# Performance work log

Measured on AMD Instinct MI355X. Metric: run time of the kernel, lower is better.

The kernel has to match this reference:

```python
import jax, jax.numpy as jnp
import numpy as np

MAX_WAVELENGTH = 10000
BIG_NEG = -2.3819763e38

def _rope(x, positions):
    # x: [B, L, H, D], positions: [B, L] float32
    d = x.shape[-1]
    freq_exp = 2.0 / d * jnp.arange(d // 2, dtype=jnp.float32)
    timescale = MAX_WAVELENGTH ** freq_exp
    radians = (positions[..., None] / timescale[None, None, :])[..., None, :]  # [B,L,1,D/2]
    sin, cos = jnp.sin(radians), jnp.cos(radians)
    x1, x2 = jnp.split(x, 2, axis=-1)
    return jnp.concatenate([x1 * cos - x2 * sin, x2 * cos + x1 * sin], axis=-1).astype(x.dtype)

def _adaln_rmsnorm(x, cond, Wmod, bmod):
    # RMSNorm in fp32, then AdaLN scale/shift; returns (normed, gate[B,1,D])
    var = jnp.mean(jnp.square(x.astype(jnp.float32)), axis=-1, keepdims=True)
    normed = x * jax.lax.rsqrt(var + 1e-6)
    mod = (cond @ Wmod + bmod)[:, None, :]  # [B,1,3D]
    scale, shift, gate = jnp.split(mod, 3, axis=-1)
    return (normed * (1 + scale) + shift).astype(x.dtype), gate

def setup_inputs() -> dict:
    key = jax.random.key(0)
    ks = jax.random.split(key, 9)
    B, T, D, F, N, K, H = 2, 2048, 2048, 16384, 8, 1, 256
    x = jax.random.normal(ks[0], (B, T, D), jnp.float32)
    positions = jnp.broadcast_to(jnp.arange(T, dtype=jnp.float32), (B, T))
    attn_mask = jnp.broadcast_to(jnp.tril(jnp.ones((T, T), dtype=bool))[None, None], (B, 1, T, T))
    cond = jax.random.normal(ks[1], (B, D), jnp.float32)
    Wmod_a = jax.random.normal(ks[2], (D, 3 * D), jnp.float32) * 0.02
    bmod_a = jnp.zeros((3 * D,), jnp.float32)
    Wq = jax.random.normal(ks[3], (N, D, H), jnp.float32) * (D ** -0.5)
    Wkv = jax.random.normal(ks[4], (2, K, D, H), jnp.float32) * (D ** -0.5)
    Wo = jax.random.normal(ks[5], (N, H, D), jnp.float32) * ((N * H) ** -0.5)
    Wmod_f = jax.random.normal(ks[6], (D, 3 * D), jnp.float32) * 0.02
    bmod_f = jnp.zeros((3 * D,), jnp.float32)
    Wg = jax.random.normal(ks[7], (2, D, F), jnp.float32) * (D ** -0.5)
    Wl = jax.random.normal(ks[8], (F, D), jnp.float32) * (F ** -0.5)
    return dict(x=x, positions=positions, attn_mask=attn_mask, cond=cond,
                Wmod_a=Wmod_a, bmod_a=bmod_a, Wq=Wq, Wkv=Wkv, Wo=Wo,
                Wmod_f=Wmod_f, bmod_f=bmod_f, Wg=Wg, Wl=Wl)

def reference(x, positions, attn_mask, cond, Wmod_a, bmod_a, Wq, Wkv, Wo, Wmod_f, bmod_f, Wg, Wl):
    K = Wkv.shape[1]               # num_kv_heads
    H = Wq.shape[-1]               # head_dim
    # --- pre-attention AdaLN RMSNorm ---
    n, gate_a = _adaln_rmsnorm(x, cond, Wmod_a, bmod_a)
    # --- GQA projections ---
    q = jnp.einsum('BTD,NDH->BTNH', n, Wq)
    k = jnp.einsum('BSD,KDH->BSKH', n, Wkv[0])
    v = jnp.einsum('BSD,KDH->BSKH', n, Wkv[1])
    q = _rope(q, positions) * (H ** -0.5)
    k = _rope(k, positions)
    B, T, N, _ = q.shape
    q = q.reshape(B, T, K, N // K, H)  # B T K G H
    logits = jnp.einsum('BTKGH,BSKH->BKGTS', q, k, preferred_element_type=jnp.float32)
    masked = jnp.where(attn_mask[:, :, None, :, :], logits, BIG_NEG)
    probs = jax.nn.softmax(masked, axis=-1).astype(x.dtype)
    enc = jnp.einsum('BKGTS,BSKH->BTKGH', probs, v).reshape(B, T, N, H)
    attn_out = jnp.einsum('BTNH,NHD->BTD', enc, Wo)
    # gated residual
    x = x + attn_out * gate_a
    # --- pre-FFN AdaLN RMSNorm + gated-GeLU MLP ---
    n, gate_f = _adaln_rmsnorm(x, cond, Wmod_f, bmod_f)
    h = jax.nn.gelu(jnp.einsum('BTD,DF->BTF', n, Wg[0])) * jnp.einsum('BTD,DF->BTF', n, Wg[1])
    mlp_out = jnp.einsum('BTF,FD->BTD', h, Wl)
    return x + mlp_out * gate_f
```

## Files before the change

### kernel.cpp

```cpp
#include <hip/hip_runtime.h>
#include <hip/hip_bf16.h>

typedef __bf16 bf16_t;
typedef __bf16 bf16x8 __attribute__((ext_vector_type(8)));
typedef float  f32x4  __attribute__((ext_vector_type(4)));

#define DEV static __device__ __forceinline__

DEV void gload16(const bf16_t* g, bf16_t* l) {
    __builtin_amdgcn_global_load_lds(
        (const __attribute__((address_space(1))) void*)g,
        (__attribute__((address_space(3))) void*)l, 16, 0, 0);
}

enum { EPI_F32 = 0, EPI_BF16 = 1, EPI_RES = 2, EPI_GELU = 3, EPI_MUL = 4 };

#define G_MFMA(d, a, b) d = __builtin_amdgcn_mfma_f32_16x16x32_bf16(a, b, d, 0, 0, 0)

#define COMPUTE(AB0, AB1, BB0, BB1)                                           \
  { bf16x8 aF[8], bF[4];                                                      \
    _Pragma("unroll") for (int m8 = 0; m8 < 8; m8++)                          \
      aF[m8] = *(const bf16x8*)(AB0 + (m8 >> 2) * 4096 + (m8 & 3) * 1024);    \
    _Pragma("unroll") for (int nj = 0; nj < 4; nj++)                          \
      bF[nj] = *(const bf16x8*)(BB0 + nj * 1024);                             \
    _Pragma("unroll") for (int m8 = 0; m8 < 8; m8++)                          \
      _Pragma("unroll") for (int nj = 0; nj < 4; nj++)                        \
        G_MFMA(acc[m8][nj], aF[m8], bF[nj]);                                  \
    _Pragma("unroll") for (int m8 = 0; m8 < 8; m8++)                          \
      aF[m8] = *(const bf16x8*)(AB1 + (m8 >> 2) * 4096 + (m8 & 3) * 1024);    \
    _Pragma("unroll") for (int nj = 0; nj < 4; nj++)                          \
      bF[nj] = *(const bf16x8*)(BB1 + nj * 1024);                             \
    _Pragma("unroll") for (int m8 = 0; m8 < 8; m8++)                          \
      _Pragma("unroll") for (int nj = 0; nj < 4; nj++)                        \
        G_MFMA(acc[m8][nj], aF[m8], bF[nj]);                                  \
  }

#define STAGE8(kt, bi)                                                        \
  { SCA(kt, bi, 0); SCA(kt, bi, 1); SCA(kt, bi, 2); SCA(kt, bi, 3);           \
    SCB(kt, bi, 0); SCB(kt, bi, 1); SCB(kt, bi, 2); SCB(kt, bi, 3); }

template<int EPI>
__global__ __launch_bounds__(512, 1)
void gemma(const bf16_t* __restrict__ A, const bf16_t* __restrict__ Bt,
           void* __restrict__ Cout, int Kd, int lda, int ldb, int ldc,
           long sCz,
           const float* __restrict__ res, const float* __restrict__ gate,
           int gateStride, int rowsPerB, const bf16_t* __restrict__ aux)
{
    const int nbx = gridDim.x;
    const int nwg = nbx * gridDim.y;
    int lin = blockIdx.y * nbx + blockIdx.x;
    const int q8 = nwg >> 3, r8 = nwg & 7;
    const int xcd = lin & 7, oo = lin >> 3;
    lin = (xcd < r8 ? xcd * (q8 + 1) : r8 * (q8 + 1) + (xcd - r8) * q8) + oo;
    const long m0 = (long)(lin / nbx) * 256;
    const long n0 = (long)(lin % nbx) * 256;
    const long kb = (long)blockIdx.z * Kd;

    const int tid = threadIdx.x;
    const int l   = tid & 63;
    const int w   = tid >> 6;
    const int wr  = w >> 2;
    const int wcn = w & 3;

    __shared__ bf16_t sA[2][16384];
    __shared__ bf16_t sB[2][16384];

    const long sgc = (long)(((l & 7) ^ (l >> 3)) << 3);
    const int NT = Kd >> 6;
    const int NI = NT >> 1;

    const bf16_t* pA0 = A + (m0 + 0 * 64 + w * 8 + (l >> 3)) * (long)lda + kb + sgc;
    const bf16_t* pA1 = A + (m0 + 1 * 64 + w * 8 + (l >> 3)) * (long)lda + kb + sgc;
    const bf16_t* pA2 = A + (m0 + 2 * 64 + w * 8 + (l >> 3)) * (long)lda + kb + sgc;
    const bf16_t* pA3 = A + (m0 + 3 * 64 + w * 8 + (l >> 3)) * (long)lda + kb + sgc;
    const bf16_t* pB0 = Bt + (n0 + 0 * 64 + w * 8 + (l >> 3)) * (long)ldb + kb + sgc;
    const bf16_t* pB1 = Bt + (n0 + 1 * 64 + w * 8 + (l >> 3)) * (long)ldb + kb + sgc;
    const bf16_t* pB2 = Bt + (n0 + 2 * 64 + w * 8 + (l >> 3)) * (long)ldb + kb + sgc;
    const bf16_t* pB3 = Bt + (n0 + 3 * 64 + w * 8 + (l >> 3)) * (long)ldb + kb + sgc;

#define SCA(kt, bi, c) gload16(pA##c + (kt), &sA[bi][(c) * 4096 + w * 512])
#define SCB(kt, bi, c) gload16(pB##c + (kt), &sB[bi][(c) * 4096 + w * 512])

    f32x4 acc[8][4];
#pragma unroll
    for (int i = 0; i < 8; i++)
#pragma unroll
        for (int j = 0; j < 4; j++) acc[i][j] = f32x4{0.f, 0.f, 0.f, 0.f};

    const int co0 = ((l >> 4) ^ (l & 7)) << 3;
    const int co1 = ((4 + (l >> 4)) ^ (l & 7)) << 3;

    const bf16_t* rbA00 = &sA[0][(wr * 128 + (l & 15)) * 64 + co0];
    const bf16_t* rbA01 = &sA[0][(wr * 128 + (l & 15)) * 64 + co1];
    const bf16_t* rbA10 = &sA[1][(wr * 128 + (l & 15)) * 64 + co0];
    const bf16_t* rbA11 = &sA[1][(wr * 128 + (l & 15)) * 64 + co1];
    const bf16_t* rbB00 = &sB[0][(wcn * 64 + (l & 15)) * 64 + co0];
    const bf16_t* rbB01 = &sB[0][(wcn * 64 + (l & 15)) * 64 + co1];
    const bf16_t* rbB10 = &sB[1][(wcn * 64 + (l & 15)) * 64 + co0];
    const bf16_t* rbB11 = &sB[1][(wcn * 64 + (l & 15)) * 64 + co1];

    STAGE8(0, 0);

    for (int it = 0; it < NI; ++it) {
        const int v = 2 * it + 1;
        asm volatile("s_waitcnt lgkmcnt(0)" ::: "memory");
        __builtin_amdgcn_s_barrier();
        STAGE8((long)v * 64, 1);
        asm volatile("s_waitcnt vmcnt(8)" ::: "memory");
        __builtin_amdgcn_s_barrier();
        COMPUTE(rbA00, rbA01, rbB00, rbB01);
        asm volatile("s_waitcnt lgkmcnt(0)" ::: "memory");
        __builtin_amdgcn_s_barrier();
        if (v + 1 < NT) {
            STAGE8((long)(v + 1) * 64, 0);
            asm volatile("s_waitcnt vmcnt(8)" ::: "memory");
        } else {
            asm volatile("s_waitcnt vmcnt(0)" ::: "memory");
        }
        __builtin_amdgcn_s_barrier();
        COMPUTE(rbA10, rbA11, rbB10, rbB11);
    }

#pragma unroll
    for (int mi = 0; mi < 8; mi++) {
#pragma unroll
        for (int nj = 0; nj < 4; nj++) {
            f32x4 vv = acc[mi][nj];
            const long col   = n0 + wcn * 64 + nj * 16 + (l & 15);
            const long row0r = m0 + wr * 128 + mi * 16 + ((l >> 4) * 4);
#pragma unroll
            for (int e = 0; e < 4; e++) {
                const long row = row0r + e;
                const long idx = row * (long)ldc + col + (long)blockIdx.z * sCz;
                const float val = vv[e];
                if constexpr (EPI == EPI_F32) {
                    ((float*)Cout)[idx] = val;
                } else if constexpr (EPI == EPI_BF16) {
                    ((bf16_t*)Cout)[idx] = (bf16_t)val;
                } else if constexpr (EPI == EPI_RES) {
                    const int b = (int)(row / rowsPerB);
                    ((float*)Cout)[idx] = res[row * (long)ldc + col] + val * gate[(long)b * gateStride + col];
                } else if constexpr (EPI == EPI_GELU) {
                    const float gl = 0.5f * val * (1.f + tanhf(0.7978845608f * (val + 0.044715f * val * val * val)));
                    ((bf16_t*)Cout)[idx] = (bf16_t)gl;
                } else if constexpr (EPI == EPI_MUL) {
                    ((bf16_t*)Cout)[idx] = (bf16_t)((float)aux[idx] * val);
                }
            }
        }
    }
#undef SCA
#undef SCB
}

__global__ __launch_bounds__(256)
void combine_splitk(const float* __restrict__ P, const float* __restrict__ res,
                    const float* __restrict__ gate, float* __restrict__ out,
                    int D, int T, int gateStride, long zstride, long n4)
{
    for (long i4 = (long)blockIdx.x * 256 + threadIdx.x; i4 < n4; i4 += (long)gridDim.x * 256) {
        const long i = i4 * 4;
        const float4 p0 = *(const float4*)(P + i);
        const float4 p1 = *(const float4*)(P + i + zstride);
        const float4 xv = *(const float4*)(res + i);
        const long row = i / D;
        const int  b   = (int)(row / T);
        const int  col = (int)(i - row * D);
        const float* gp = gate + (long)b * gateStride + col;
        float4 r;
        r.x = xv.x + (p0.x + p1.x) * gp[0];
        r.y = xv.y + (p0.y + p1.y) * gp[1];
        r.z = xv.z + (p0.z + p1.z) * gp[2];
        r.w = xv.w + (p0.w + p1.w) * gp[3];
        *(float4*)(out + i) = r;
    }
}

template<int EPI, int CAUSAL>
__global__ __launch_bounds__(256)
void gemm_bt(const bf16_t* __restrict__ A, const bf16_t* __restrict__ Bt,
             void* __restrict__ Cout,
             int M, int N, int Kd, int lda, int ldb, int ldc,
             long sAz, long sBz, long sCz, long sCz2)
{
    const int tid = threadIdx.x;
    const int l   = tid & 63;
    const int w   = tid >> 6;
    const int wr  = w >> 1, wc = w & 1;
    const long m0 = (long)blockIdx.y * 128;
    const long n0 = (long)blockIdx.x * 128;
    const int  z  = blockIdx.z;

    if constexpr (CAUSAL == 1) {
        if (n0 > m0 + 127) return;
    }
    int kend = Kd;
    if constexpr (CAUSAL == 2) {
        const int kc = (int)m0 + 128;
        kend = kc < Kd ? kc : Kd;
    }

    A  += (long)z * sAz;
    Bt += (long)(z >> 3) * sBz;
    const long cOff = (long)(z >> 3) * sCz2 + (long)(z & 7) * sCz;

    __shared__ bf16_t As[128 * 32];
    __shared__ bf16_t Bs[128 * 32];

    const int srow = w * 16 + (l >> 2);
    const int scol = (l & 3) * 8;
    const bf16_t* Ag = A  + (m0 + srow) * (long)lda + scol;
    const bf16_t* Bg = Bt + (n0 + srow) * (long)ldb + scol;

    bf16_t* ldsA = As + w * 512;
    bf16_t* ldsB = Bs + w * 512;

    f32x4 acc[16];
    const f32x4 fz = {0.f, 0.f, 0.f, 0.f};
#pragma unroll
    for (int i = 0; i < 16; i++) acc[i] = fz;

    for (int k0 = 0; k0 < kend; k0 += 32) {
        gload16(Ag + k0,                  ldsA);
        gload16(Ag + k0 + 64 * (long)lda, ldsA + 2048);
        gload16(Bg + k0,                  ldsB);
        gload16(Bg + k0 + 64 * (long)ldb, ldsB + 2048);
        __syncthreads();

        bf16x8 af[4], bfr[4];
#pragma unroll
        for (int f = 0; f < 4; f++) {
            af[f]  = *(const bf16x8*)(As + (wr * 64 + f * 16 + (l & 15)) * 32 + (l >> 4) * 8);
            bfr[f] = *(const bf16x8*)(Bs + (wc * 64 + f * 16 + (l & 15)) * 32 + (l >> 4) * 8);
        }
#pragma unroll
        for (int i = 0; i < 4; i++)
#pragma unroll
            for (int j = 0; j < 4; j++)
                acc[i * 4 + j] = __builtin_amdgcn_mfma_f32_16x16x32_bf16(af[i], bfr[j], acc[i * 4 + j], 0, 0, 0);
        __syncthreads();
    }

#pragma unroll
    for (int i = 0; i < 4; i++) {
#pragma unroll
        for (int j = 0; j < 4; j++) {
            f32x4 v = acc[i * 4 + j];
            const long col  = n0 + wc * 64 + j * 16 + (l & 15);
            const long row0 = m0 + wr * 64 + i * 16 + ((l >> 4) * 4);
#pragma unroll
            for (int e = 0; e < 4; e++) {
                const long row = row0 + e;
                const long idx = row * (long)ldc + col + cOff;
                ((bf16_t*)Cout)[idx] = (bf16_t)v[e];
            }
        }
    }
}

__global__ __launch_bounds__(256)
void transpose_f2b(const float* __restrict__ in, bf16_t* __restrict__ out,
                   int R, int C, long inStride, long outStride)
{
    __shared__ float tile[32][33];
    in  += (long)blockIdx.z * inStride;
    out += (long)blockIdx.z * outStride;
    const int c0 = blockIdx.x * 32, r0 = blockIdx.y * 32;
    const int tx = threadIdx.x, ty = threadIdx.y;
#pragma unroll
    for (int i = 0; i < 4; i++)
        tile[ty + i * 8][tx] = in[(long)(r0 + ty + i * 8) * C + c0 + tx];
    __syncthreads();
#pragma unroll
    for (int i = 0; i < 4; i++)
        out[(long)(c0 + ty + i * 8) * R + r0 + tx] = (bf16_t)tile[tx][ty + i * 8];
}

__global__ __launch_bounds__(256)
void modk_part(const float* __restrict__ cond, const float* __restrict__ W,
               float* __restrict__ part, int D3, int KS)
{
    const int j = blockIdx.x * 256 + threadIdx.x;
    const int b = blockIdx.y;
    const int z = blockIdx.z;
    const float* cb = cond + (long)b * (KS * gridDim.z);
    float s = 0.f;
    const int d0 = z * KS;
#pragma unroll 4
    for (int d = d0; d < d0 + KS; d++) s += cb[d] * W[(long)d * D3 + j];
    part[((long)z * gridDim.y + b) * D3 + j] = s;
}

__global__ __launch_bounds__(256)
void modk_reduce(const float* __restrict__ part, const float* __restrict__ bvec,
                 float* __restrict__ mod, int D3, int NZ)
{
    const int j = blockIdx.x * 256 + threadIdx.x;
    const int b = blockIdx.y;
    float s = bvec[j];
    for (int z = 0; z < NZ; z++) s += part[((long)z * gridDim.y + b) * D3 + j];
    mod[(long)b * D3 + j] = s;
}

__global__ __launch_bounds__(256)
void rmsnorm_adaln(const float* __restrict__ xin, const float* __restrict__ mod,
                   bf16_t* __restrict__ out, int D, int T, int D3)
{
    const long row = blockIdx.x;
    const int  b   = (int)(row / T);
    const int  tid = threadIdx.x;
    const float4* x4 = (const float4*)(xin + row * (long)D);
    const float4 v0 = x4[tid], v1 = x4[tid + 256];
    float ss = v0.x * v0.x + v0.y * v0.y + v0.z * v0.z + v0.w * v0.w
             + v1.x * v1.x + v1.y * v1.y + v1.z * v1.z + v1.w * v1.w;
    for (int o = 32; o; o >>= 1) ss += __shfl_down(ss, o, 64);
    __shared__ float red[4];
    if ((tid & 63) == 0) red[tid >> 6] = ss;
    __syncthreads();
    ss = red[0] + red[1] + red[2] + red[3];
    const float rs = rsqrtf(ss / (float)D + 1e-6f);
    const float* sc = mod + (long)b * D3;
    const float* sh = sc + D;
    const float4 s0 = ((const float4*)sc)[tid], s1 = ((const float4*)sc)[tid + 256];
    const float4 h0 = ((const float4*)sh)[tid], h1 = ((const float4*)sh)[tid + 256];
    bf16_t* orow = out + row * (long)D;
    orow[tid * 4 + 0]         = (bf16_t)(v0.x * rs * (1.f + s0.x) + h0.x);
    orow[tid * 4 + 1]         = (bf16_t)(v0.y * rs * (1.f + s0.y) + h0.y);
    orow[tid * 4 + 2]         = (bf16_t)(v0.z * rs * (1.f + s0.z) + h0.z);
    orow[tid * 4 + 3]         = (bf16_t)(v0.w * rs * (1.f + s0.w) + h0.w);
    orow[(tid + 256) * 4 + 0] = (bf16_t)(v1.x * rs * (1.f + s1.x) + h1.x);
    orow[(tid + 256) * 4 + 1] = (bf16_t)(v1.y * rs * (1.f + s1.y) + h1.y);
    orow[(tid + 256) * 4 + 2] = (bf16_t)(v1.z * rs * (1.f + s1.z) + h1.z);
    orow[(tid + 256) * 4 + 3] = (bf16_t)(v1.w * rs * (1.f + s1.w) + h1.w);
}

__global__ __launch_bounds__(128)
void rope_q(const bf16_t* __restrict__ qp, const float* __restrict__ positions,
            bf16_t* __restrict__ qo, int T, int ldq, int H)
{
    const int t = blockIdx.x, n = blockIdx.y, b = blockIdx.z;
    const int i = threadIdx.x;
    const long in0 = ((long)(b * T + t)) * ldq + n * H;
    const float x1 = (float)qp[in0 + i];
    const float x2 = (float)qp[in0 + i + 128];
    const float pos = positions[b * T + t];
    const float inv = expf(-9.210340371976184f * (float)i / 128.f);
    float s, c;
    sincosf(pos * inv, &s, &c);
    const float scl = 0.0625f;
    const long out0 = (((long)(b * 8 + n)) * T + t) * H;
    qo[out0 + i]       = (bf16_t)((x1 * c - x2 * s) * scl);
    qo[out0 + i + 128] = (bf16_t)((x2 * c + x1 * s) * scl);
}

__global__ __launch_bounds__(128)
void rope_kv(const bf16_t* __restrict__ kvp, const float* __restrict__ positions,
             bf16_t* __restrict__ ko, bf16_t* __restrict__ vt, int T, int H, int S, int ldkv)
{
    const int t = blockIdx.x, b = blockIdx.y;
    const int i = threadIdx.x;
    const long in0 = ((long)(b * T + t)) * ldkv;
    const float k1 = (float)kvp[in0 + i];
    const float k2 = (float)kvp[in0 + i + 128];
    const float pos = positions[b * T + t];
    const float inv = expf(-9.210340371976184f * (float)i / 128.f);
    float s, c;
    sincosf(pos * inv, &s, &c);
    const long ko0 = ((long)(b * T + t)) * H;
    ko[ko0 + i]       = (bf16_t)(k1 * c - k2 * s);
    ko[ko0 + i + 128] = (bf16_t)(k2 * c + k1 * s);
    vt[((long)b * H + i) * S + t]       = kvp[in0 + 256 + i];
    vt[((long)b * H + i + 128) * S + t] = kvp[in0 + 256 + i + 128];
}

__global__ __launch_bounds__(256)
void softmax_causal(bf16_t* __restrict__ sc, int T, int S)
{
    const int t = blockIdx.x, z = blockIdx.y;
    const long row = (long)z * T + t;
    bf16_t* srow = sc + row * S;
    const int tid = threadIdx.x;
    const int limit = t | 127;
    const int nch = (limit >> 8) + 1;
    float vals[8];
    float mx = -3.4e38f;
    for (int i = 0; i < nch; i++) {
        const int s = i * 256 + tid;
        const float v = (s <= t) ? (float)srow[s] : -3.4e38f;
        vals[i] = v;
        mx = fmaxf(mx, v);
    }
    for (int o = 32; o; o >>= 1) mx = fmaxf(mx, __shfl_down(mx, o, 64));
    __shared__ float red[4];
    if ((tid & 63) == 0) red[tid >> 6] = mx;
    __syncthreads();
    mx = fmaxf(fmaxf(red[0], red[1]), fmaxf(red[2], red[3]));
    __syncthreads();
    float sum = 0.f;
    for (int i = 0; i < nch; i++) {
        const int s = i * 256 + tid;
        const float e = (s <= t) ? __expf(vals[i] - mx) : 0.f;
        vals[i] = e;
        sum += e;
    }
    for (int o = 32; o; o >>= 1) sum += __shfl_down(sum, o, 64);
    if ((tid & 63) == 0) red[tid >> 6] = sum;
    __syncthreads();
    sum = red[0] + red[1] + red[2] + red[3];
    const float invs = 1.f / sum;
    for (int i = 0; i < nch; i++)
        srow[i * 256 + tid] = (bf16_t)(vals[i] * invs);
}

extern "C" void kernel_launch(void* const* d_in, const int* in_sizes, int n_in,
                              void* d_out, int out_size, void* d_ws, size_t ws_size,
                              hipStream_t stream)
{
    const float* x      = (const float*)d_in[0];
    const float* pos    = (const float*)d_in[1];
    const float* cond   = (const float*)d_in[3];
    const float* Wmod_a = (const float*)d_in[4];
    const float* bmod_a = (const float*)d_in[5];
    const float* Wq     = (const float*)d_in[6];
    const float* Wkv    = (const float*)d_in[7];
    const float* Wo     = (const float*)d_in[8];
    const float* Wmod_f = (const float*)d_in[9];
    const float* bmod_f = (const float*)d_in[10];
    const float* Wg     = (const float*)d_in[11];
    const float* Wl     = (const float*)d_in[12];

    constexpr int  Bb = 2, T = 2048, D = 2048, F = 16384, Nh = 8, H = 256;
    constexpr int  NH = 2048, S = 2048, BT = 4096, D3 = 6144;
    constexpr int  KSLICE = 64, NZ = D / KSLICE;
    constexpr int  NQKV = 2560;

    char* ws = (char*)d_ws;
    size_t off = 0;
    auto alloc = [&](size_t bytes) { char* p = ws + off; off += bytes; return p; };

    bf16_t* WQT  = (bf16_t*)alloc((size_t)NH * D * 2);
    bf16_t* WKVT = (bf16_t*)alloc((size_t)512 * D * 2);
    bf16_t* WOT  = (bf16_t*)alloc((size_t)D * NH * 2);
    bf16_t* WGT  = (bf16_t*)alloc((size_t)2 * F * D * 2);
    bf16_t* WLT  = (bf16_t*)alloc((size_t)D * F * 2);
    float*  MODA = (float*)alloc((size_t)Bb * D3 * 4);
    float*  MODF = (float*)alloc((size_t)Bb * D3 * 4);
    float*  PART = (float*)alloc((size_t)NZ * Bb * D3 * 4);
    bf16_t* NA   = (bf16_t*)alloc((size_t)BT * D * 2);
    bf16_t* QKVP = (bf16_t*)alloc((size_t)BT * NQKV * 2);
    bf16_t* Qr   = (bf16_t*)alloc((size_t)Bb * Nh * T * H * 2);
    bf16_t* Kr   = (bf16_t*)alloc((size_t)Bb * T * H * 2);
    bf16_t* VT   = (bf16_t*)alloc((size_t)Bb * H * S * 2);
    bf16_t* ENC  = (bf16_t*)alloc((size_t)BT * NH * 2);
    float*  X1   = (float*)alloc((size_t)BT * D * 4);
    bf16_t* NF   = (bf16_t*)alloc((size_t)BT * D * 2);
    const size_t scBytes = (size_t)16 * T * S * 2;
    const size_t hBytes  = (size_t)BT * F * 2;
    const size_t headBytes = (scBytes > hBytes) ? scBytes : hBytes;
    char* big = alloc(headBytes + (size_t)2 * BT * D * 4);
    bf16_t* SCb   = (bf16_t*)big;
    bf16_t* Hb    = (bf16_t*)big;
    float*  PARTK = (float*)(big + headBytes);
    (void)ws_size; (void)in_sizes; (void)n_in; (void)out_size;

    const dim3 tb(32, 8);
    transpose_f2b<<<dim3(H / 32, D / 32, 8), tb, 0, stream>>>(Wq,  WQT,  D,  H, (long)D * H, (long)H * D);
    transpose_f2b<<<dim3(H / 32, D / 32, 2), tb, 0, stream>>>(Wkv, WKVT, D,  H, (long)D * H, (long)H * D);
    transpose_f2b<<<dim3(D / 32, NH / 32, 1), tb, 0, stream>>>(Wo, WOT, NH,  D, 0, 0);
    transpose_f2b<<<dim3(F / 32, D / 32, 2), tb, 0, stream>>>(Wg,  WGT,  D,  F, (long)D * F, (long)F * D);
    transpose_f2b<<<dim3(D / 32, F / 32, 1), tb, 0, stream>>>(Wl,  WLT,  F,  D, 0, 0);
    modk_part<<<dim3(D3 / 256, Bb, NZ), 256, 0, stream>>>(cond, Wmod_a, PART, D3, KSLICE);
    modk_reduce<<<dim3(D3 / 256, Bb), 256, 0, stream>>>(PART, bmod_a, MODA, D3, NZ);
    modk_part<<<dim3(D3 / 256, Bb, NZ), 256, 0, stream>>>(cond, Wmod_f, PART, D3, KSLICE);
    modk_reduce<<<dim3(D3 / 256, Bb), 256, 0, stream>>>(PART, bmod_f, MODF, D3, NZ);
    rmsnorm_adaln<<<BT, 256, 0, stream>>>(x, MODA, NA, D, T, D3);
    gemma<EPI_BF16><<<dim3(NQKV / 256, BT / 256, 1), 512, 0, stream>>>(
        NA, WQT, QKVP, D, D, D, NQKV, 0, nullptr, nullptr, 0, 0, nullptr);
    rope_q<<<dim3(T, Nh, Bb), 128, 0, stream>>>(QKVP, pos, Qr, T, NQKV, H);
    rope_kv<<<dim3(T, Bb), 128, 0, stream>>>(QKVP + NH, pos, Kr, VT, T, H, S, NQKV);
    gemm_bt<EPI_BF16, 1><<<dim3(S / 128, T / 128, 16), 256, 0, stream>>>(
        Qr, Kr, SCb, T, S, H, H, H, S,
        (long)T * H, (long)T * H, (long)T * S, 8L * T * S);
    softmax_causal<<<dim3(T, 16), 256, 0, stream>>>(SCb, T, S);
    gemm_bt<EPI_BF16, 2><<<dim3(H / 128, T / 128, 16), 256, 0, stream>>>(
        SCb, VT, ENC, T, H, S, S, S, NH,
        (long)T * S, (long)H * S, (long)H, (long)T * NH);
    gemma<EPI_F32><<<dim3(D / 256, BT / 256, 2), 512, 0, stream>>>(
        ENC, WOT, PARTK, NH / 2, NH, NH, D, (long)BT * D, nullptr, nullptr, 0, 0, nullptr);
    combine_splitk<<<2048, 256, 0, stream>>>(
        PARTK, x, MODA + 2 * D, X1, D, T, D3, (long)BT * D, (long)BT * D / 4);
    rmsnorm_adaln<<<BT, 256, 0, stream>>>(X1, MODF, NF, D, T, D3);
    gemma<EPI_GELU><<<dim3(F / 256, BT / 256, 1), 512, 0, stream>>>(
        NF, WGT, Hb, D, D, D, F, 0, nullptr, nullptr, 0, 0, nullptr);
    gemma<EPI_MUL><<<dim3(F / 256, BT / 256, 1), 512, 0, stream>>>(
        NF, WGT + (long)F * D, Hb, D, D, D, F, 0, nullptr, nullptr, 0, 0, Hb);
    gemma<EPI_F32><<<dim3(D / 256, BT / 256, 2), 512, 0, stream>>>(
        Hb, WLT, PARTK, F / 2, F, F, D, (long)BT * D, nullptr, nullptr, 0, 0, nullptr);
    combine_splitk<<<2048, 256, 0, stream>>>(
        PARTK, X1, MODF + 2 * D, (float*)d_out, D, T, D3, (long)BT * D, (long)BT * D / 4);
}
```

Measured before the change: 1.470 ms.

## Triple-buffer B tiles to prefetch B two stages ahead in GEMM

Restructures the GEMM main loop so the B operand is triple-buffered in LDS and loaded two K-tiles ahead, while A stays double-buffered and one tile ahead. The loop is unrolled by six so the buffer indices rotate statically, with a simple unpipelined tail for the remaining tiles. This is meant to hide more global-load latency behind MFMA work. In exchange it uses more LDS (a third B buffer) and adds a serialized remainder loop when the tile count is not a multiple of six.

Measured after the change: 1.485 ms. Within noise of the previous version (+1.0%).

```diff
diff --git a/kernel.cpp b/kernel.cpp
--- a/kernel.cpp
+++ b/kernel.cpp
@@ -35,9 +35,19 @@
         G_MFMA(acc[m8][nj], aF[m8], bF[nj]);                                  \
   }
 
-#define STAGE8(kt, bi)                                                        \
-  { SCA(kt, bi, 0); SCA(kt, bi, 1); SCA(kt, bi, 2); SCA(kt, bi, 3);           \
-    SCB(kt, bi, 0); SCB(kt, bi, 1); SCB(kt, bi, 2); SCB(kt, bi, 3); }
+#define STAGEA(kt, bi) { SCA(kt, bi, 0); SCA(kt, bi, 1); SCA(kt, bi, 2); SCA(kt, bi, 3); }
+#define STAGEB(kt, bi) { SCB(kt, bi, 0); SCB(kt, bi, 1); SCB(kt, bi, 2); SCB(kt, bi, 3); }
+
+#define TILE(t, CA, CB, NA_, NB_)                                             \
+  { asm volatile("s_waitcnt lgkmcnt(0)" ::: "memory");                        \
+    __builtin_amdgcn_s_barrier();                                             \
+    if ((t) + 1 < NT6) STAGEA((long)((t) + 1) * 64, NA_);                     \
+    if ((t) + 2 < NT6) STAGEB((long)((t) + 2) * 64, NB_);                     \
+    if ((t) + 3 <= NT6)      { asm volatile("s_waitcnt vmcnt(12)" ::: "memory"); } \
+    else if ((t) + 2 == NT6) { asm volatile("s_waitcnt vmcnt(8)"  ::: "memory"); } \
+    else                     { asm volatile("s_waitcnt vmcnt(0)"  ::: "memory"); } \
+    __builtin_amdgcn_s_barrier();                                             \
+    COMPUTE(rbA##CA##0, rbA##CA##1, rbB##CB##0, rbB##CB##1); }
 
 template<int EPI>
 __global__ __launch_bounds__(512, 1)
@@ -64,11 +74,11 @@
     const int wcn = w & 3;
 
     __shared__ bf16_t sA[2][16384];
-    __shared__ bf16_t sB[2][16384];
+    __shared__ bf16_t sB[3][16384];
 
     const long sgc = (long)(((l & 7) ^ (l >> 3)) << 3);
-    const int NT = Kd >> 6;
-    const int NI = NT >> 1;
+    const int NT  = Kd >> 6;
+    const int NT6 = NT - (NT % 6);
 
     const bf16_t* pA0 = A + (m0 + 0 * 64 + w * 8 + (l >> 3)) * (long)lda + kb + sgc;
     const bf16_t* pA1 = A + (m0 + 1 * 64 + w * 8 + (l >> 3)) * (long)lda + kb + sgc;
@@ -99,27 +109,33 @@
     const bf16_t* rbB01 = &sB[0][(wcn * 64 + (l & 15)) * 64 + co1];
     const bf16_t* rbB10 = &sB[1][(wcn * 64 + (l & 15)) * 64 + co0];
     const bf16_t* rbB11 = &sB[1][(wcn * 64 + (l & 15)) * 64 + co1];
-
-    STAGE8(0, 0);
-
-    for (int it = 0; it < NI; ++it) {
-        const int v = 2 * it + 1;
+    const bf16_t* rbB20 = &sB[2][(wcn * 64 + (l & 15)) * 64 + co0];
+    const bf16_t* rbB21 = &sB[2][(wcn * 64 + (l & 15)) * 64 + co1];
+
+    if (NT6 >= 6) {
+        STAGEA(0, 0);
+        STAGEB(0, 0);
+        STAGEB(64, 1);
+        asm volatile("s_waitcnt vmcnt(4)" ::: "memory");
+        __builtin_amdgcn_s_barrier();
+
+        for (int tb = 0; tb < NT6; tb += 6) {
+            TILE(tb + 0, 0, 0, 1, 2)
+            TILE(tb + 1, 1, 1, 0, 0)
+            TILE(tb + 2, 0, 2, 1, 1)
+            TILE(tb + 3, 1, 0, 0, 2)
+            TILE(tb + 4, 0, 1, 1, 0)
+            TILE(tb + 5, 1, 2, 0, 1)
+        }
+    }
+    for (int t = NT6; t < NT; ++t) {
         asm volatile("s_waitcnt lgkmcnt(0)" ::: "memory");
         __builtin_amdgcn_s_barrier();
-        STAGE8((long)v * 64, 1);
-        asm volatile("s_waitcnt vmcnt(8)" ::: "memory");
+        STAGEA((long)t * 64, 0);
+        STAGEB((long)t * 64, 0);
+        asm volatile("s_waitcnt vmcnt(0)" ::: "memory");
         __builtin_amdgcn_s_barrier();
         COMPUTE(rbA00, rbA01, rbB00, rbB01);
-        asm volatile("s_waitcnt lgkmcnt(0)" ::: "memory");
-        __builtin_amdgcn_s_barrier();
-        if (v + 1 < NT) {
-            STAGE8((long)(v + 1) * 64, 0);
-            asm volatile("s_waitcnt vmcnt(8)" ::: "memory");
-        } else {
-            asm volatile("s_waitcnt vmcnt(0)" ::: "memory");
-        }
-        __builtin_amdgcn_s_barrier();
-        COMPUTE(rbA10, rbA11, rbB10, rbB11);
     }
 
 #pragma unroll
```
